# Kernel optimization log

Measured on AMD Instinct MI355X. Metric: run time of the kernel, lower is better.

The kernel has to match this reference:

```python
import jax, jax.numpy as jnp
import numpy as np

N_NODES = 50000
N_EDGES = 800000
D_IN = 128
D_OUT = 128


def setup_inputs() -> dict:
    key = jax.random.key(0)
    k1, k2, k3, k4, k5 = jax.random.split(key, 5)
    feature = jax.random.normal(k1, (N_NODES, D_IN), dtype=jnp.float32)
    src = jax.random.randint(k2, (N_EDGES,), 0, N_NODES, dtype=jnp.int32)
    dst = jax.random.randint(k3, (N_EDGES,), 0, N_NODES, dtype=jnp.int32)
    # nn.Linear-style init: U(-1/sqrt(in), 1/sqrt(in))
    bound = 1.0 / np.sqrt(D_IN)
    W = jax.random.uniform(k4, (D_OUT, D_IN), minval=-bound, maxval=bound, dtype=jnp.float32)
    b = jax.random.uniform(k5, (D_OUT,), minval=-bound, maxval=bound, dtype=jnp.float32)
    return {"feature": feature, "src": src, "dst": dst, "W": W, "b": b}


def reference(feature, src, dst, W, b):
    # copy_src: gather source node features along edges, then sum-reduce per dst
    msgs = feature[src]                                    # [E, D_IN]
    h = jax.ops.segment_sum(msgs, dst, num_segments=N_NODES)  # [N, D_IN]
    # linear projection: h @ W^T + b
    return jnp.einsum("nd,od->no", h, W) + b               # [N, D_OUT]
```

## Files before the change

kernel.cpp:

```cpp
#include <hip/hip_runtime.h>
#include <hip/hip_bf16.h>


#define BKT_SHIFT 7
#define MAX_BKT   512
#define NPART     128
#define CAP       2432
#define NCAP      96

typedef __attribute__((ext_vector_type(8))) short short8;
typedef __attribute__((ext_vector_type(4))) float float4v;

__device__ __forceinline__ unsigned short f2bf_rne(float f) {
    unsigned int u = __float_as_uint(f);
    u += 0x7FFFu + ((u >> 16) & 1u);
    return (unsigned short)(u >> 16);
}

__global__ __launch_bounds__(256) void conv_scatter_kernel(
    const float* __restrict__ feat, const float* __restrict__ W,
    unsigned short* __restrict__ out_bf, long nf, long nw,
    const int* __restrict__ src, const int* __restrict__ dst,
    int* __restrict__ cursor, int2* __restrict__ pairs,
    int n_edges, int nb, int chunk)
{
    if ((int)blockIdx.x < NPART) {
        __shared__ int lcnt[MAX_BKT];
        __shared__ int lcur[MAX_BKT];
        int tid = threadIdx.x;
        int p   = blockIdx.x;
        int e0  = p * chunk;
        int e1  = min(e0 + chunk, n_edges);

        for (int i = tid; i < nb; i += 256) lcnt[i] = 0;
        __syncthreads();
        for (int e = e0 + tid; e < e1; e += 256)
            atomicAdd(&lcnt[dst[e] >> BKT_SHIFT], 1);
        __syncthreads();
        for (int i = tid; i < nb; i += 256) {
            int c = lcnt[i];
            int base = c ? atomicAdd(&cursor[i], c) : 0;
            lcur[i] = i * CAP + base;
        }
        __syncthreads();
        for (int e = e0 + tid; e < e1; e += 256) {
            int d = dst[e];
            int s = src[e];
            int pos = atomicAdd(&lcur[d >> BKT_SHIFT], 1);
            pairs[pos] = make_int2(d, s);
        }
    } else {
        long i4 = ((long)(blockIdx.x - NPART) * 256 + threadIdx.x) * 4;
        if (i4 >= nf + nw) return;
        const float* srcp = (i4 < nf) ? (feat + i4) : (W + (i4 - nf));
        float4 v = *(const float4*)srcp;
        ushort4 o;
        o.x = f2bf_rne(v.x); o.y = f2bf_rne(v.y);
        o.z = f2bf_rne(v.z); o.w = f2bf_rne(v.w);
        *(ushort4*)(out_bf + i4) = o;
    }
}

#define HT_STRIDE 136

#define ACC8(U)                                                     \
    do {                                                            \
        acc[0] += __uint_as_float((U).x << 16);                     \
        acc[1] += __uint_as_float((U).x & 0xFFFF0000u);             \
        acc[2] += __uint_as_float((U).y << 16);                     \
        acc[3] += __uint_as_float((U).y & 0xFFFF0000u);             \
        acc[4] += __uint_as_float((U).z << 16);                     \
        acc[5] += __uint_as_float((U).z & 0xFFFF0000u);             \
        acc[6] += __uint_as_float((U).w << 16);                     \
        acc[7] += __uint_as_float((U).w & 0xFFFF0000u);             \
    } while (0)

__global__ __launch_bounds__(1024, 8) void gcn_gather_mm_kernel(
    const unsigned short* __restrict__ feat_bf,
    const int2* __restrict__ pairs, const int* __restrict__ cursor,
    const unsigned short* __restrict__ w_bf, const float* __restrict__ bias,
    float* __restrict__ out, int n_nodes)
{
    __shared__ unsigned short htile[16 * HT_STRIDE];
    __shared__ int list[16][NCAP];
    __shared__ int lcnt[16];

    int tid   = threadIdx.x;
    int lane  = tid & 63;
    int w     = tid >> 6;
    int node0 = blockIdx.x * 16;
    int node  = node0 + w;
    int sub   = lane >> 4;
    int c16   = lane & 15;

    int bucket = node0 >> BKT_SHIFT;
    int bstart = bucket * CAP;
    int bcnt   = cursor[bucket];

    if (tid < 16) lcnt[tid] = 0;
    __syncthreads();
    for (int i = tid; i < bcnt; i += 1024) {
        int2 pr = pairs[bstart + i];
        int local = pr.x - node0;
        if ((unsigned)local < 16u) {
            int pos = atomicAdd(&lcnt[local], 1);
            if (pos < NCAP) list[local][pos] = pr.y;
        }
    }
    __syncthreads();

    float acc[8];
    #pragma unroll
    for (int j = 0; j < 8; j++) acc[j] = 0.f;

    int deg = (node < n_nodes) ? min(lcnt[w], NCAP) : 0;
    if (deg > 0) {
        const unsigned short* colp = feat_bf + c16 * 8;
        const int* lst = &list[w][0];

        for (int base = 0; base < deg; base += 64) {
            int nch = min(64, deg - base);
            int sv = 0;
            if (base + lane < deg) sv = lst[base + lane];

            int g = 0;
            for (; g + 16 <= nch; g += 16) {
                int sa = __shfl(sv, g + sub);
                int sb = __shfl(sv, g + 4 + sub);
                int sc = __shfl(sv, g + 8 + sub);
                int sd = __shfl(sv, g + 12 + sub);
                uint4 ua = *(const uint4*)(colp + (size_t)sa * 128);
                uint4 ub = *(const uint4*)(colp + (size_t)sb * 128);
                uint4 uc = *(const uint4*)(colp + (size_t)sc * 128);
                uint4 ud = *(const uint4*)(colp + (size_t)sd * 128);
                ACC8(ua); ACC8(ub); ACC8(uc); ACC8(ud);
            }
            for (; g + 4 <= nch; g += 4) {
                int s0 = __shfl(sv, g + sub);
                uint4 u = *(const uint4*)(colp + (size_t)s0 * 128);
                ACC8(u);
            }
            if (g < nch) {
                int rem = nch - g;
                int idx = g + (sub < rem ? sub : rem - 1);
                int s = __shfl(sv, idx);
                uint4 u = *(const uint4*)(colp + (size_t)s * 128);
                if (sub < rem) ACC8(u);
            }
        }
        #pragma unroll
        for (int j = 0; j < 8; j++) {
            acc[j] += __shfl_xor(acc[j], 16);
            acc[j] += __shfl_xor(acc[j], 32);
        }
    }

    if (sub == 0) {
        short8 o;
        #pragma unroll
        for (int j = 0; j < 8; j++) o[j] = (short)f2bf_rne(acc[j]);
        *(short8*)(htile + w * HT_STRIDE + c16 * 8) = o;
    }

    __syncthreads();

    if (w < 8) {
        int m = lane & 15;
        int q = lane >> 4;

        float4v accd = {0.f, 0.f, 0.f, 0.f};
        #pragma unroll
        for (int kk = 0; kk < 4; kk++) {
            short8 afrag = *(const short8*)(htile + m * HT_STRIDE + kk * 32 + q * 8);
            short8 bfrag = *(const short8*)(w_bf + (size_t)(w * 16 + m) * 128 + kk * 32 + q * 8);
            accd = __builtin_amdgcn_mfma_f32_16x16x32_bf16(afrag, bfrag, accd, 0, 0, 0);
        }
        float bv = bias[w * 16 + m];
        #pragma unroll
        for (int r = 0; r < 4; r++) {
            int row = node0 + q * 4 + r;
            if (row < n_nodes)
                out[(size_t)row * 128 + w * 16 + m] = accd[r] + bv;
        }
    }
}

extern "C" void kernel_launch(void* const* d_in, const int* in_sizes, int n_in,
                              void* d_out, int out_size, void* d_ws, size_t ws_size,
                              hipStream_t stream) {
    const float* feature = (const float*)d_in[0];
    const int*   src     = (const int*)d_in[1];
    const int*   dst     = (const int*)d_in[2];
    const float* W       = (const float*)d_in[3];
    const float* b       = (const float*)d_in[4];

    const int D  = 128;
    int n_nodes  = in_sizes[0] / D;
    int n_edges  = in_sizes[1];
    int nb       = (n_nodes + 127) >> BKT_SHIFT;

    float* out = (float*)d_out;

    long nf = (long)n_nodes * D;
    long nw = (long)D * D;

    unsigned short* bf_base    = (unsigned short*)d_ws;
    unsigned short* feature_bf = bf_base;
    unsigned short* w_bf       = bf_base + nf;
    int2* pairs   = (int2*)(bf_base + nf + nw);
    int*  cursor  = (int*)(pairs + (size_t)nb * CAP);

    int chunk = (n_edges + NPART - 1) / NPART;

    hipMemsetAsync(cursor, 0, (size_t)nb * sizeof(int), stream);

    {
        long conv_blocks = ((nf + nw) / 4 + 255) / 256;
        int grid = NPART + (int)conv_blocks;
        conv_scatter_kernel<<<grid, 256, 0, stream>>>(
            feature, W, bf_base, nf, nw, src, dst, cursor, pairs,
            n_edges, nb, chunk);
    }

    {
        int blocks = (n_nodes + 15) / 16;
        gcn_gather_mm_kernel<<<blocks, 1024, 0, stream>>>(
            feature_bf, pairs, cursor, w_bf, b, out, n_nodes);
    }
}
```

Baseline: 152.9 us.

## Pack edge pairs into 32-bit words and vectorize scatter with wider blocks

Each edge record shrinks from an int2 (dst, src) to one 32-bit word holding the 7-bit local dst offset and a 20-bit src index. This halves the pairs traffic written by the scatter and re-read by the gather. The scatter phase also reads dst/src as int4 vectors and the conversion/scatter kernel moves to 512-thread blocks. The packing assumes node ids fit in 20 bits, which holds for 50k nodes but caps graph size. The int4 loads assume each chunk start is 16-byte aligned.

```diff
diff --git a/kernel.cpp b/kernel.cpp
--- a/kernel.cpp
+++ b/kernel.cpp
@@ -17,11 +17,11 @@
     return (unsigned short)(u >> 16);
 }
 
-__global__ __launch_bounds__(256) void conv_scatter_kernel(
+__global__ __launch_bounds__(512) void conv_scatter_kernel(
     const float* __restrict__ feat, const float* __restrict__ W,
     unsigned short* __restrict__ out_bf, long nf, long nw,
     const int* __restrict__ src, const int* __restrict__ dst,
-    int* __restrict__ cursor, int2* __restrict__ pairs,
+    int* __restrict__ cursor, unsigned int* __restrict__ pairs,
     int n_edges, int nb, int chunk)
 {
     if ((int)blockIdx.x < NPART) {
@@ -31,26 +31,46 @@
         int p   = blockIdx.x;
         int e0  = p * chunk;
         int e1  = min(e0 + chunk, n_edges);
-
-        for (int i = tid; i < nb; i += 256) lcnt[i] = 0;
+        int cnt = e1 - e0;
+        int nfull = cnt >> 2;
+
+        for (int i = tid; i < nb; i += 512) lcnt[i] = 0;
         __syncthreads();
-        for (int e = e0 + tid; e < e1; e += 256)
+        for (int k = tid; k < nfull; k += 512) {
+            int4 d4 = *(const int4*)(dst + e0 + k * 4);
+            atomicAdd(&lcnt[d4.x >> BKT_SHIFT], 1);
+            atomicAdd(&lcnt[d4.y >> BKT_SHIFT], 1);
+            atomicAdd(&lcnt[d4.z >> BKT_SHIFT], 1);
+            atomicAdd(&lcnt[d4.w >> BKT_SHIFT], 1);
+        }
+        for (int e = e0 + nfull * 4 + tid; e < e1; e += 512)
             atomicAdd(&lcnt[dst[e] >> BKT_SHIFT], 1);
         __syncthreads();
-        for (int i = tid; i < nb; i += 256) {
+        for (int i = tid; i < nb; i += 512) {
             int c = lcnt[i];
             int base = c ? atomicAdd(&cursor[i], c) : 0;
             lcur[i] = i * CAP + base;
         }
         __syncthreads();
-        for (int e = e0 + tid; e < e1; e += 256) {
+        for (int k = tid; k < nfull; k += 512) {
+            int4 d4 = *(const int4*)(dst + e0 + k * 4);
+            int4 s4 = *(const int4*)(src + e0 + k * 4);
+            int p0 = atomicAdd(&lcur[d4.x >> BKT_SHIFT], 1);
+            pairs[p0] = ((unsigned)(d4.x & 127) << 20) | (unsigned)s4.x;
+            int p1 = atomicAdd(&lcur[d4.y >> BKT_SHIFT], 1);
+            pairs[p1] = ((unsigned)(d4.y & 127) << 20) | (unsigned)s4.y;
+            int p2 = atomicAdd(&lcur[d4.z >> BKT_SHIFT], 1);
+            pairs[p2] = ((unsigned)(d4.z & 127) << 20) | (unsigned)s4.z;
+            int p3 = atomicAdd(&lcur[d4.w >> BKT_SHIFT], 1);
+            pairs[p3] = ((unsigned)(d4.w & 127) << 20) | (unsigned)s4.w;
+        }
+        for (int e = e0 + nfull * 4 + tid; e < e1; e += 512) {
             int d = dst[e];
-            int s = src[e];
             int pos = atomicAdd(&lcur[d >> BKT_SHIFT], 1);
-            pairs[pos] = make_int2(d, s);
+            pairs[pos] = ((unsigned)(d & 127) << 20) | (unsigned)src[e];
         }
     } else {
-        long i4 = ((long)(blockIdx.x - NPART) * 256 + threadIdx.x) * 4;
+        long i4 = ((long)(blockIdx.x - NPART) * 512 + threadIdx.x) * 4;
         if (i4 >= nf + nw) return;
         const float* srcp = (i4 < nf) ? (feat + i4) : (W + (i4 - nf));
         float4 v = *(const float4*)srcp;
@@ -77,7 +97,7 @@
 
 __global__ __launch_bounds__(1024, 8) void gcn_gather_mm_kernel(
     const unsigned short* __restrict__ feat_bf,
-    const int2* __restrict__ pairs, const int* __restrict__ cursor,
+    const unsigned int* __restrict__ pairs, const int* __restrict__ cursor,
     const unsigned short* __restrict__ w_bf, const float* __restrict__ bias,
     float* __restrict__ out, int n_nodes)
 {
@@ -93,18 +113,19 @@
     int sub   = lane >> 4;
     int c16   = lane & 15;
 
-    int bucket = node0 >> BKT_SHIFT;
-    int bstart = bucket * CAP;
-    int bcnt   = cursor[bucket];
+    int bucket   = node0 >> BKT_SHIFT;
+    int bstart   = bucket * CAP;
+    int bcnt     = cursor[bucket];
+    int sub_base = node0 & 127;
 
     if (tid < 16) lcnt[tid] = 0;
     __syncthreads();
     for (int i = tid; i < bcnt; i += 1024) {
-        int2 pr = pairs[bstart + i];
-        int local = pr.x - node0;
+        unsigned int pr = pairs[bstart + i];
+        int local = (int)(pr >> 20) - sub_base;
         if ((unsigned)local < 16u) {
             int pos = atomicAdd(&lcnt[local], 1);
-            if (pos < NCAP) list[local][pos] = pr.y;
+            if (pos < NCAP) list[local][pos] = (int)(pr & 0xFFFFFu);
         }
     }
     __syncthreads();
@@ -207,17 +228,17 @@
     unsigned short* bf_base    = (unsigned short*)d_ws;
     unsigned short* feature_bf = bf_base;
     unsigned short* w_bf       = bf_base + nf;
-    int2* pairs   = (int2*)(bf_base + nf + nw);
-    int*  cursor  = (int*)(pairs + (size_t)nb * CAP);
+    unsigned int* pairs  = (unsigned int*)(bf_base + nf + nw);
+    int*          cursor = (int*)(pairs + (size_t)nb * CAP);
 
     int chunk = (n_edges + NPART - 1) / NPART;
 
     hipMemsetAsync(cursor, 0, (size_t)nb * sizeof(int), stream);
 
     {
-        long conv_blocks = ((nf + nw) / 4 + 255) / 256;
+        long conv_blocks = ((nf + nw) / 4 + 511) / 512;
         int grid = NPART + (int)conv_blocks;
-        conv_scatter_kernel<<<grid, 256, 0, stream>>>(
+        conv_scatter_kernel<<<grid, 512, 0, stream>>>(
             feature, W, bf_base, nf, nw, src, dst, cursor, pairs,
             n_edges, nb, chunk);
     }
```

Result: faster. 143.7 us (-6.0%).
